# Kernel tuning notes

Hardware: AMD Instinct MI355X
Metric: run time of the kernel (lower is better)

The kernel has to match this reference:

```python
import jax, jax.numpy as jnp
import numpy as np

B, H, W, C = 2, 64, 64, 1024
L = H * W
HC, WC = 32, 32
NH, DH = 16, 64
NUM_REMAIN = 1638


def setup_inputs() -> dict:
    key = jax.random.key(0)
    ks = jax.random.split(key, 8)
    s = 1.0 / np.sqrt(C)
    x = jax.random.normal(ks[0], (B, L, C), jnp.float32)
    cached_x = jax.random.normal(ks[1], (B, HC, WC, C), jnp.float32)
    W_qkv = jax.random.normal(ks[2], (3 * C, C), jnp.float32) * s
    q_bias = jnp.zeros((C,), jnp.float32)
    v_bias = jnp.zeros((C,), jnp.float32)
    W_proj = jax.random.normal(ks[3], (C, C), jnp.float32) * s
    b_proj = jnp.zeros((C,), jnp.float32)
    scale_mul_log = jnp.full((1, NH, 1, 1), np.log(4.0), jnp.float32)
    # rope cache as (cos, sin) pairs over the flat token axis, DH//2 freqs
    ang = jax.random.uniform(ks[4], (L, DH // 2), jnp.float32) * (2 * np.pi)
    rope_grid = jnp.stack([jnp.cos(ang), jnp.sin(ang)], axis=0)  # (2, L, DH//2)
    return {"x": x, "cached_x": cached_x, "W_qkv": W_qkv, "q_bias": q_bias,
            "v_bias": v_bias, "W_proj": W_proj, "b_proj": b_proj,
            "scale_mul_log": scale_mul_log, "rope_grid": rope_grid,
            "num_remain": NUM_REMAIN}


def reference(x, cached_x, W_qkv, q_bias, v_bias, W_proj, b_proj,
              scale_mul_log, rope_grid, num_remain):
    Bx, Lx, Cx = x.shape
    # --- FastVAR token merge: MSE-to-spatial-mean selection (adaptive_avg_pool2d -> mean over L)
    mean_x = jnp.mean(x, axis=1, keepdims=True)                      # (B,1,C)
    mse = jnp.sum((x - mean_x) ** 2, axis=-1)                        # (B,L)
    idx = jnp.argsort(-mse, axis=1)[:, :num_remain]                  # (B,n) descending
    bix = jnp.arange(Bx)[:, None]
    xm = x[bix, idx]                                                 # (B,n,C) merged tokens
    # --- qkv projection with (q_bias, 0, v_bias)
    bias = jnp.concatenate([q_bias, jnp.zeros_like(q_bias), v_bias])
    qkv = (xm @ W_qkv.T + bias).reshape(Bx, -1, 3, NH, DH)
    qkv = qkv.transpose(2, 0, 3, 1, 4)                               # (3,B,H,n,dh)
    q, k, v = qkv[0], qkv[1], qkv[2]
    # --- cos attention: L2-normalize q,k; head-wise learned scale on q; sdpa scale = 1
    scale_mul = jnp.exp(jnp.minimum(scale_mul_log, jnp.log(100.0)))  # (1,NH,1,1)
    def l2n(t):
        return t / jnp.maximum(jnp.linalg.norm(t, axis=-1, keepdims=True), 1e-12)
    q = l2n(q) * scale_mul
    k = l2n(k)
    # --- 2D RoPE with per-sample gathered cache at the kept-token positions
    rc = rope_grid[:, idx, :]                                        # (2,B,n,DH//2)
    r0 = rc[0][:, None, :, :]                                        # (B,1,n,DH//2)
    r1 = rc[1][:, None, :, :]
    def rope(t):
        tp = t.reshape(*t.shape[:-1], DH // 2, 2)
        t0, t1 = tp[..., 0], tp[..., 1]
        return jnp.stack([r0 * t0 - r1 * t1, r1 * t0 + r0 * t1], axis=-1).reshape(t.shape)
    q = rope(q)
    k = rope(k)
    # --- attention over merged tokens
    attn = jax.nn.softmax(jnp.einsum('bhqd,bhkd->bhqk', q, k), axis=-1)
    o = jnp.einsum('bhqk,bhkd->bhqd', attn, v)                       # (B,H,n,dh)
    o = o.transpose(0, 2, 1, 3).reshape(Bx, -1, Cx)                  # (B,n,C)
    o = o @ W_proj.T + b_proj
    up = jnp.repeat(jnp.repeat(cached_x, 2, axis=1), 2, axis=2).reshape(Bx, Lx, Cx)
    out_full = up.at[bix, idx].set(o)
    return x + out_full
```

## Files before the change

kernel.cpp:

```cpp
#include <hip/hip_runtime.h>
#include <hip/hip_bf16.h>
#include <math.h>

#define BQ   2
#define LQ   4096
#define CQ   1024
#define NHQ  16
#define DHQ  64
#define KSEL 1638
#define KPAD 1664
#define MTOT (BQ*KSEL)
#define MPAD 3328

typedef short s16x8 __attribute__((ext_vector_type(8)));
typedef float fx4   __attribute__((ext_vector_type(4)));

#define MFMA16(a,b,c) __builtin_amdgcn_mfma_f32_16x16x32_bf16(a,b,c,0,0,0)

__device__ __forceinline__ float b2f(unsigned short u) {
  union { float f; unsigned int i; } cv; cv.i = ((unsigned int)u) << 16; return cv.f;
}
__device__ __forceinline__ unsigned short f2b(float f) {
  union { float f; unsigned int i; } cv; cv.f = f;
  unsigned int x = cv.i;
  return (unsigned short)((x + 0x7fffu + ((x >> 16) & 1u)) >> 16);
}
__device__ __forceinline__ unsigned int fbits(float f) {
  union { float f; unsigned int i; } cv; cv.f = f; return cv.i;
}
__device__ __forceinline__ void async16(const void* g, void* l) {
  __builtin_amdgcn_global_load_lds((const __attribute__((address_space(1))) void*)g,
                                   (__attribute__((address_space(3))) void*)l, 16, 0, 0);
}
__device__ __forceinline__ float fexp2(float x) {
#if __has_builtin(__builtin_amdgcn_exp2f)
  return __builtin_amdgcn_exp2f(x);
#else
  return __expf(x * 0.69314718055994531f);
#endif
}

__global__ __launch_bounds__(256) void k_cvt2(const float* __restrict__ wqkv,
                                              const float* __restrict__ wproj,
                                              unsigned short* __restrict__ wqb,
                                              unsigned short* __restrict__ wpb) {
  int i = blockIdx.x * 256 + threadIdx.x;
  const float* s; unsigned short* d; int off;
  if (i < 786432) { s = wqkv;  d = wqb; off = i; }
  else            { s = wproj; d = wpb; off = i - 786432; }
  float4 v = ((const float4*)s)[off];
  ushort4 o;
  o.x = f2b(v.x); o.y = f2b(v.y); o.z = f2b(v.z); o.w = f2b(v.w);
  ((ushort4*)d)[off] = o;
}

__global__ __launch_bounds__(256) void k_mean_part(const float* __restrict__ x,
                                                   double* __restrict__ part) {
  int bid = blockIdx.x;
  int cb = bid & 3, ch = (bid >> 2) & 31, b = bid >> 7;
  int c = cb * 256 + threadIdx.x;
  const float* p = x + ((size_t)b * LQ + (size_t)ch * 128) * CQ + c;
  double s = 0.0;
  for (int r = 0; r < 128; ++r) s += (double)p[(size_t)r * CQ];
  part[((size_t)b * 32 + ch) * CQ + c] = s;
}

__global__ __launch_bounds__(256) void k_mean_reduce(const double* __restrict__ part,
                                                     double* __restrict__ mean) {
  int g = blockIdx.x * 256 + threadIdx.x;
  int b = g >> 10, c = g & 1023;
  double s = 0.0;
  for (int ch = 0; ch < 32; ++ch) s += part[((size_t)b * 32 + ch) * CQ + c];
  mean[g] = s * (1.0 / 4096.0);
}

__global__ __launch_bounds__(256) void k_mse_base(const float* __restrict__ x,
                                                  const float* __restrict__ cached,
                                                  const double* __restrict__ mean,
                                                  double* __restrict__ mse,
                                                  float* __restrict__ out,
                                                  unsigned short* __restrict__ xb) {
  int bl = blockIdx.x; int b = bl >> 12, l = bl & 4095;
  int hh = l >> 6, ww = l & 63;
  size_t xoff = ((size_t)b * LQ + l) * CQ;
  size_t uoff = (((size_t)b * 32 + (hh >> 1)) * 32 + (ww >> 1)) * CQ;
  const double* mrow = mean + (size_t)b * CQ;
  int c0 = threadIdx.x * 4;
  float4 xv = *(const float4*)(x + xoff + c0);
  float4 uv = *(const float4*)(cached + uoff + c0);
  float4 ov;
  ov.x = xv.x + uv.x; ov.y = xv.y + uv.y; ov.z = xv.z + uv.z; ov.w = xv.w + uv.w;
  *(float4*)(out + xoff + c0) = ov;
  ushort4 xo;
  xo.x = f2b(xv.x); xo.y = f2b(xv.y); xo.z = f2b(xv.z); xo.w = f2b(xv.w);
  ((ushort4*)xb)[(xoff + c0) >> 2] = xo;
  double d0 = (double)xv.x - mrow[c0];
  double d1 = (double)xv.y - mrow[c0 + 1];
  double d2 = (double)xv.z - mrow[c0 + 2];
  double d3 = (double)xv.w - mrow[c0 + 3];
  double ss = d0 * d0 + d1 * d1 + d2 * d2 + d3 * d3;
  for (int o = 1; o < 64; o <<= 1) ss += __shfl_xor(ss, o);
  __shared__ double ws4[4];
  if ((threadIdx.x & 63) == 0) ws4[threadIdx.x >> 6] = ss;
  __syncthreads();
  if (threadIdx.x == 0) mse[(size_t)b * LQ + l] = ws4[0] + ws4[1] + ws4[2] + ws4[3];
}

__global__ __launch_bounds__(1024) void k_topk(const double* __restrict__ mse,
                                               int* __restrict__ idx_sel) {
  __shared__ unsigned long long u[4096];
  __shared__ unsigned int whist[16 * 257];
  __shared__ unsigned int wtot[4];
  __shared__ unsigned long long sh_prefix;
  __shared__ int sh_rem, sh_rem2, sh_bsel, sh_cnt, sh_eqcnt;
  __shared__ int eqbuf[256];
  int b = blockIdx.x, t = threadIdx.x;
  int wv = t >> 6, laneid = t & 63;
  for (int p = 0; p < 4; ++p) {
    int i = p * 1024 + t;
    u[i] = (unsigned long long)__double_as_longlong(mse[(size_t)b * LQ + i]);
  }
  if (t == 0) { sh_prefix = 0ULL; sh_rem = KSEL; sh_cnt = 0; sh_eqcnt = 0; }
  __syncthreads();
  for (int shift = 56; shift >= 0; shift -= 8) {
    for (int z = t; z < 16 * 257; z += 1024) whist[z] = 0u;
    __syncthreads();
    unsigned long long pref = sh_prefix;
#pragma unroll
    for (int p = 0; p < 4; ++p) {
      int i = p * 1024 + t;
      unsigned long long v = u[i];
      bool cand = (shift == 56) || ((v >> ((shift + 8) & 63)) == pref);
      if (cand) atomicAdd(&whist[wv * 257 + ((unsigned int)(v >> shift) & 255u)], 1u);
    }
    __syncthreads();
    unsigned int myc = 0, mysc = 0;
    if (t < 256) {
      unsigned int s = 0;
      int bin = 255 - t;
#pragma unroll
      for (int wvi = 0; wvi < 16; ++wvi) s += whist[wvi * 257 + bin];
      myc = s;
      mysc = myc;
#pragma unroll
      for (int o = 1; o < 64; o <<= 1) {
        unsigned int v2 = __shfl_up(mysc, o);
        if (laneid >= o) mysc += v2;
      }
      if (laneid == 63) wtot[wv] = mysc;
    }
    __syncthreads();
    if (t < 256) {
      unsigned int basep = 0;
      for (int wvi = 0; wvi < wv; ++wvi) basep += wtot[wvi];
      unsigned int incl = basep + mysc;
      unsigned int excl = incl - myc;
      unsigned int rem = (unsigned int)sh_rem;
      if (excl < rem && rem <= incl) {
        sh_bsel = 255 - t;
        sh_rem2 = (int)(rem - excl);
      }
    }
    __syncthreads();
    if (t == 0) {
      sh_prefix = (sh_prefix << 8) | (unsigned long long)sh_bsel;
      sh_rem = sh_rem2;
    }
    __syncthreads();
  }
  unsigned long long T = sh_prefix;
  int rem_eq = sh_rem;
#pragma unroll
  for (int p = 0; p < 4; ++p) {
    int i = p * 1024 + t;
    unsigned long long v = u[i];
    bool win = (v > T);
    unsigned long long mask = __ballot(win);
    int total = __popcll(mask);
    int base = 0;
    if (laneid == 0 && total > 0) base = atomicAdd(&sh_cnt, total);
    base = __shfl(base, 0);
    if (win) {
      int lpos = __popcll(mask & ((1ULL << laneid) - 1ULL));
      idx_sel[b * KPAD + base + lpos] = i;
    }
    if (v == T) {
      int e = atomicAdd(&sh_eqcnt, 1);
      if (e < 256) eqbuf[e] = i;
    }
  }
  __syncthreads();
  if (t == 0) {
    int n = sh_eqcnt; if (n > 256) n = 256;
    for (int a = 1; a < n; ++a) {
      int key = eqbuf[a]; int c = a - 1;
      while (c >= 0 && eqbuf[c] > key) { eqbuf[c + 1] = eqbuf[c]; --c; }
      eqbuf[c + 1] = key;
    }
    int base = sh_cnt;
    for (int a = 0; a < rem_eq && a < n; ++a) idx_sel[b * KPAD + base + a] = eqbuf[a];
    for (int a = KSEL; a < KPAD; ++a) idx_sel[b * KPAD + a] = 0;
  }
}

__global__ __launch_bounds__(256) void k_gemmA(const unsigned short* __restrict__ Asrc,
                                               const unsigned short* __restrict__ Bmat,
                                               const int* __restrict__ idx_sel,
                                               unsigned short* __restrict__ Cbf) {
  int bm = blockIdx.x % 26, bn = blockIdx.x / 26;
  int tid = threadIdx.x;
  int w = tid >> 6, lane = tid & 63, quad = lane >> 4, l15 = lane & 15;
  int wm = w & 1, wn = w >> 1;
  __shared__ __align__(16) unsigned char sm[2][16384];

  const unsigned short* gA[2];
  const unsigned short* gB[2];
#pragma unroll
  for (int p = 0; p < 2; ++p) {
    int e = p * 256 + tid; int row = e >> 2, kc = e & 3;
    int m = bm * 128 + row; if (m >= MTOT) m = MTOT - 1;
    int bb = m / KSEL; int ii = m - bb * KSEL;
    int lsel = idx_sel[bb * KPAD + ii];
    gA[p] = Asrc + ((size_t)bb * LQ + lsel) * CQ + kc * 8;
    gB[p] = Bmat + (size_t)(bn * 128 + row) * CQ + kc * 8;
  }

  fx4 acc[4][4];
#pragma unroll
  for (int a = 0; a < 4; ++a)
#pragma unroll
    for (int c = 0; c < 4; ++c) acc[a][c] = (fx4){0.f, 0.f, 0.f, 0.f};

#define STAGE_A(buf, it) do { int ke = (it) * 32;                                   \
    _Pragma("unroll")                                                               \
    for (int p = 0; p < 2; ++p) {                                                   \
      async16(gA[p] + ke, sm[buf] + p * 4096 + w * 1024);                           \
      async16(gB[p] + ke, sm[buf] + 8192 + p * 4096 + w * 1024);                    \
    } } while (0)

  STAGE_A(0, 0);
  for (int it = 0; it < 32; ++it) {
    int cur = it & 1;
    if (it < 31) STAGE_A(cur ^ 1, it + 1);
    if (it < 31) asm volatile("s_waitcnt vmcnt(4)");
    else         asm volatile("s_waitcnt vmcnt(0)");
    __builtin_amdgcn_s_barrier();
    const unsigned char* smb = sm[cur];
    s16x8 af[4], bf[4];
#pragma unroll
    for (int mt = 0; mt < 4; ++mt)
      af[mt] = *(const s16x8*)(smb + ((wm * 64 + mt * 16 + l15) * 64 + quad * 16));
#pragma unroll
    for (int nt = 0; nt < 4; ++nt)
      bf[nt] = *(const s16x8*)(smb + 8192 + ((wn * 64 + nt * 16 + l15) * 64 + quad * 16));
#pragma unroll
    for (int mt = 0; mt < 4; ++mt)
#pragma unroll
      for (int nt = 0; nt < 4; ++nt)
        acc[mt][nt] = MFMA16(af[mt], bf[nt], acc[mt][nt]);
    __builtin_amdgcn_s_barrier();
  }
#undef STAGE_A

#pragma unroll
  for (int mt = 0; mt < 4; ++mt)
#pragma unroll
    for (int nt = 0; nt < 4; ++nt) {
      int n = bn * 128 + wn * 64 + nt * 16 + l15;
      int mbase = bm * 128 + wm * 64 + mt * 16 + quad * 4;
      fx4 vv = acc[mt][nt];
#pragma unroll
      for (int r = 0; r < 4; ++r) {
        int m = mbase + r;
        if (m < MTOT) Cbf[(size_t)m * 3072 + n] = f2b(vv[r]);
      }
    }
}

__global__ __launch_bounds__(256) void k_gemmB(const unsigned short* __restrict__ Asrc,
                                               const unsigned short* __restrict__ Bmat,
                                               const int* __restrict__ idx_sel,
                                               float* __restrict__ Cf,
                                               const float* __restrict__ xin,
                                               const float* __restrict__ bproj) {
  int bid = blockIdx.x;
  int swz = (bid & 7) * 104 + (bid >> 3);
  int bm = swz % 52, bn = swz / 52;
  int tid = threadIdx.x;
  int w = tid >> 6, lane = tid & 63, quad = lane >> 4, l15 = lane & 15;
  int wm = w & 1, wn = w >> 1;
  __shared__ __align__(16) unsigned char sm[2][16384];

  const unsigned short* g4[4];
#pragma unroll
  for (int p = 0; p < 4; ++p) {
    int e = (p & 1) * 256 + tid; int row = e >> 3, kc = e & 7;
    if (p < 2) {
      int m = bm * 64 + row; if (m >= MTOT) m = MTOT - 1;
      int bb = m / KSEL; int ii = m - bb * KSEL;
      g4[p] = Asrc + ((size_t)bb * KPAD + ii) * CQ + kc * 8;
    } else {
      g4[p] = Bmat + (size_t)(bn * 64 + row) * CQ + kc * 8;
    }
  }

  fx4 acc[2][2];
#pragma unroll
  for (int a = 0; a < 2; ++a)
#pragma unroll
    for (int c = 0; c < 2; ++c) acc[a][c] = (fx4){0.f, 0.f, 0.f, 0.f};

#define STAGE_B(buf, it) do { int ke = (it) * 64;                                   \
    _Pragma("unroll")                                                               \
    for (int p = 0; p < 4; ++p)                                                     \
      async16(g4[p] + ke, sm[buf] + p * 4096 + w * 1024);                           \
    } while (0)

  STAGE_B(0, 0);
  for (int it = 0; it < 16; ++it) {
    int cur = it & 1;
    if (it < 15) STAGE_B(cur ^ 1, it + 1);
    if (it < 15) asm volatile("s_waitcnt vmcnt(4)");
    else         asm volatile("s_waitcnt vmcnt(0)");
    __builtin_amdgcn_s_barrier();
    const unsigned char* smb = sm[cur];
#pragma unroll
    for (int kk = 0; kk < 2; ++kk) {
      s16x8 af[2], bf2[2];
#pragma unroll
      for (int mt = 0; mt < 2; ++mt)
        af[mt] = *(const s16x8*)(smb + ((wm * 32 + mt * 16 + l15) * 64 + kk * 32 + quad * 8) * 2);
#pragma unroll
      for (int nt = 0; nt < 2; ++nt)
        bf2[nt] = *(const s16x8*)(smb + 8192 + ((wn * 32 + nt * 16 + l15) * 64 + kk * 32 + quad * 8) * 2);
#pragma unroll
      for (int mt = 0; mt < 2; ++mt)
#pragma unroll
        for (int nt = 0; nt < 2; ++nt)
          acc[mt][nt] = MFMA16(af[mt], bf2[nt], acc[mt][nt]);
    }
    __builtin_amdgcn_s_barrier();
  }
#undef STAGE_B

#pragma unroll
  for (int mt = 0; mt < 2; ++mt)
#pragma unroll
    for (int nt = 0; nt < 2; ++nt) {
      int n = bn * 64 + wn * 32 + nt * 16 + l15;
      int mbase = bm * 64 + wm * 32 + mt * 16 + quad * 4;
      fx4 vv = acc[mt][nt];
      float bp = bproj[n];
#pragma unroll
      for (int r = 0; r < 4; ++r) {
        int m = mbase + r;
        if (m < MTOT) {
          int bb = m / KSEL; int ii = m - bb * KSEL;
          int lsel = idx_sel[bb * KPAD + ii];
          size_t off = ((size_t)bb * LQ + lsel) * CQ + n;
          Cf[off] = xin[off] + vv[r] + bp;
        }
      }
    }
}

__global__ __launch_bounds__(256) void k_normrope(const unsigned short* __restrict__ qkv,
                                                  const int* __restrict__ idx_sel,
                                                  const float* __restrict__ qbias,
                                                  const float* __restrict__ vbias,
                                                  const float* __restrict__ sml,
                                                  const float* __restrict__ rope,
                                                  unsigned short* __restrict__ qo,
                                                  unsigned short* __restrict__ ko,
                                                  unsigned short* __restrict__ vt) {
  int bid = blockIdx.x;
  int tile = bid % 26; int h = (bid / 26) & 15; int b = bid / (26 * 16);
  int tid = threadIdx.x; int w = tid >> 6; int d = tid & 63;
  __shared__ unsigned short vtile[64 * 68];
  float scale = expf(fminf(sml[h], 4.6051702f)) * 1.4426950408889634f;
  float qb = qbias[h * 64 + d];
  float vb = vbias[h * 64 + d];
  for (int pass = 0; pass < 16; ++pass) {
    int il = pass * 4 + w;
    int i = tile * 64 + il;
    float vraw = 0.f;
    if (i < KSEL) {
      int lsel = idx_sel[b * KPAD + i];
      size_t base = ((size_t)(b * KSEL + i)) * 3072 + h * 64 + d;
      int tt = d >> 1;
      float r0 = rope[(size_t)lsel * 32 + tt];
      float r1 = rope[(size_t)LQ * 32 + (size_t)lsel * 32 + tt];
      float qv = b2f(qkv[base]) + qb;
      float ss = qv * qv;
      for (int o = 1; o < 64; o <<= 1) ss += __shfl_xor(ss, o);
      float qn = qv / fmaxf(sqrtf(ss), 1e-12f) * scale;
      float qp = __shfl_xor(qn, 1);
      float qr = (d & 1) ? (r1 * qp + r0 * qn) : (r0 * qn - r1 * qp);
      qo[((size_t)(b * NHQ + h) * KPAD + i) * 64 + d] = f2b(qr);
      float kv = b2f(qkv[base + 1024]);
      float ks = kv * kv;
      for (int o = 1; o < 64; o <<= 1) ks += __shfl_xor(ks, o);
      float kn = kv / fmaxf(sqrtf(ks), 1e-12f);
      float kp = __shfl_xor(kn, 1);
      float kr = (d & 1) ? (r1 * kp + r0 * kn) : (r0 * kn - r1 * kp);
      ko[((size_t)(b * NHQ + h) * KPAD + i) * 64 + d] = f2b(kr);
      vraw = b2f(qkv[base + 2048]) + vb;
    }
    vtile[d * 68 + il] = f2b(vraw);
  }
  __syncthreads();
  int row = tid >> 2, c0 = (tid & 3) * 16;
  s16x8 o0, o1;
#pragma unroll
  for (int jj = 0; jj < 8; ++jj) {
    o0[jj] = (short)vtile[row * 68 + c0 + jj];
    o1[jj] = (short)vtile[row * 68 + c0 + 8 + jj];
  }
  size_t doff = ((size_t)((b * NHQ + h) * 64 + row)) * KPAD + (size_t)tile * 64 + c0;
  *(s16x8*)(vt + doff) = o0;
  *(s16x8*)(vt + doff + 8) = o1;
}

__global__ __launch_bounds__(256, 4) void k_attn(const unsigned short* __restrict__ qb,
                                                 const unsigned short* __restrict__ kb,
                                                 const unsigned short* __restrict__ vtb,
                                                 const float* __restrict__ sml,
                                                 unsigned short* __restrict__ pO,
                                                 float* __restrict__ pl) {
  int qt = blockIdx.x; int bh = blockIdx.y; int part = blockIdx.z;
  int b = bh >> 4, h = bh & 15;
  int t0 = part * 13, t1 = t0 + 13;
  int q0 = qt * 128;
  int tid = threadIdx.x, w = tid >> 6, lane = tid & 63, quad = lane >> 4, l15 = lane & 15;
  float M = __expf(fminf(sml[h], 4.6051702f)) * 1.4426950408889634f;
  __shared__ __align__(16) unsigned short Kt[64 * 72];
  __shared__ __align__(16) unsigned short Vt[64 * 72];
  __shared__ __align__(16) unsigned short Pq[4][32 * 72];
  unsigned short* Pw = Pq[w];
  const unsigned short* qbase = qb + (size_t)(b * NHQ + h) * KPAD * 64;
  const unsigned short* kbase = kb + (size_t)(b * NHQ + h) * KPAD * 64;
  const unsigned short* vbase = vtb + (size_t)(b * NHQ + h) * 64 * KPAD;

  s16x8 qf[2][2];
#pragma unroll
  for (int qtile = 0; qtile < 2; ++qtile)
#pragma unroll
    for (int kb2 = 0; kb2 < 2; ++kb2) {
      int row = q0 + w * 32 + qtile * 16 + l15;
      qf[qtile][kb2] = *(const s16x8*)(qbase + (size_t)row * 64 + kb2 * 32 + quad * 8);
    }

  float lsum[2] = {0.f, 0.f};
  fx4 oacc[2][4];
#pragma unroll
  for (int qtile = 0; qtile < 2; ++qtile)
#pragma unroll
    for (int dt = 0; dt < 4; ++dt) oacc[qtile][dt] = (fx4){0.f, 0.f, 0.f, 0.f};

  for (int t = t0; t < t1; ++t) {
    int j0 = t * 64;
    bool tail = (j0 + 64 > KSEL);
    __syncthreads();
#pragma unroll
    for (int p = 0; p < 2; ++p) {
      int e = p * 256 + tid; int row = e >> 3, kc = e & 7;
      *(s16x8*)(Kt + row * 72 + kc * 8) =
          *(const s16x8*)(kbase + (size_t)(j0 + row) * 64 + kc * 8);
      *(s16x8*)(Vt + row * 72 + kc * 8) =
          *(const s16x8*)(vbase + (size_t)row * KPAD + j0 + kc * 8);
    }
    __syncthreads();

    fx4 sacc[2][4];
#pragma unroll
    for (int qtile = 0; qtile < 2; ++qtile)
#pragma unroll
      for (int jj = 0; jj < 4; ++jj) sacc[qtile][jj] = (fx4){0.f, 0.f, 0.f, 0.f};
#pragma unroll
    for (int jj = 0; jj < 4; ++jj) {
      int jl = jj * 16 + l15;
      s16x8 kf0 = *(const s16x8*)(Kt + jl * 72 + quad * 8);
      s16x8 kf1 = *(const s16x8*)(Kt + jl * 72 + 32 + quad * 8);
      sacc[0][jj] = MFMA16(kf0, qf[0][0], sacc[0][jj]);
      sacc[1][jj] = MFMA16(kf0, qf[1][0], sacc[1][jj]);
      sacc[0][jj] = MFMA16(kf1, qf[0][1], sacc[0][jj]);
      sacc[1][jj] = MFMA16(kf1, qf[1][1], sacc[1][jj]);
    }
#pragma unroll
    for (int qtile = 0; qtile < 2; ++qtile)
#pragma unroll
      for (int jj = 0; jj < 4; ++jj) {
        int jbase = j0 + jj * 16 + quad * 4;
        fx4 sv = sacc[qtile][jj];
        float p0 = fexp2(sv[0] - M);
        float p1 = fexp2(sv[1] - M);
        float p2 = fexp2(sv[2] - M);
        float p3 = fexp2(sv[3] - M);
        if (tail) {
          if (jbase + 0 >= KSEL) p0 = 0.f;
          if (jbase + 1 >= KSEL) p1 = 0.f;
          if (jbase + 2 >= KSEL) p2 = 0.f;
          if (jbase + 3 >= KSEL) p3 = 0.f;
        }
        lsum[qtile] += (p0 + p1) + (p2 + p3);
        unsigned int lo = (fbits(p1) & 0xffff0000u) | (fbits(p0) >> 16);
        unsigned int hi = (fbits(p3) & 0xffff0000u) | (fbits(p2) >> 16);
        *(uint2*)(Pw + (qtile * 16 + l15) * 72 + jj * 16 + quad * 4) =
            make_uint2(lo, hi);
      }
#pragma unroll
    for (int js = 0; js < 2; ++js) {
      s16x8 pf0 = *(const s16x8*)(Pw + l15 * 72 + js * 32 + quad * 8);
      s16x8 pf1 = *(const s16x8*)(Pw + (16 + l15) * 72 + js * 32 + quad * 8);
#pragma unroll
      for (int dt = 0; dt < 4; ++dt) {
        s16x8 vf = *(const s16x8*)(Vt + (dt * 16 + l15) * 72 + js * 32 + quad * 8);
        oacc[0][dt] = MFMA16(pf0, vf, oacc[0][dt]);
        oacc[1][dt] = MFMA16(pf1, vf, oacc[1][dt]);
      }
    }
  }

#pragma unroll
  for (int qtile = 0; qtile < 2; ++qtile) {
    float s = lsum[qtile];
    s += __shfl_xor(s, 16);
    s += __shfl_xor(s, 32);
    lsum[qtile] = s;
  }

  size_t pbase = (((size_t)part * 2 + b) * NHQ + h) * KPAD;
#pragma unroll
  for (int qtile = 0; qtile < 2; ++qtile) {
    int gqb = q0 + w * 32 + qtile * 16;
    if (quad == 0) pl[pbase + gqb + l15] = lsum[qtile];
  }

#pragma unroll
  for (int qtile = 0; qtile < 2; ++qtile)
#pragma unroll
    for (int dt = 0; dt < 4; ++dt)
#pragma unroll
      for (int r = 0; r < 4; ++r)
        Pw[(qtile * 16 + quad * 4 + r) * 72 + dt * 16 + l15] = f2b(oacc[qtile][dt][r]);
#pragma unroll
  for (int pass = 0; pass < 4; ++pass) {
    int row = pass * 8 + (lane >> 3), chunk = lane & 7;
    s16x8 vv = *(const s16x8*)(Pw + row * 72 + chunk * 8);
    *(s16x8*)(pO + (pbase + q0 + w * 32 + row) * 64 + chunk * 8) = vv;
  }
}

__global__ __launch_bounds__(256) void k_comb(const unsigned short* __restrict__ pO,
                                              const float* __restrict__ pl,
                                              unsigned short* __restrict__ ob) {
  size_t g = (size_t)blockIdx.x * 256 + threadIdx.x;
  int d = (int)(g & 63);
  size_t row = g >> 6;
  int gq = (int)(row % KPAD);
  int bhh = (int)(row / KPAD);
  int b = bhh >> 4, h = bhh & 15;
  float oa = b2f(pO[g]);
  float obv = b2f(pO[g + 3407872]);
  float la = pl[row], lb = pl[row + 53248];
  float o = (oa + obv) / (la + lb);
  ob[((size_t)(b * KPAD + gq)) * CQ + h * 64 + d] = f2b(o);
}

extern "C" void kernel_launch(void* const* d_in, const int* in_sizes, int n_in,
                              void* d_out, int out_size, void* d_ws, size_t ws_size,
                              hipStream_t stream) {
  const float* x      = (const float*)d_in[0];
  const float* cached = (const float*)d_in[1];
  const float* wqkv   = (const float*)d_in[2];
  const float* qbias  = (const float*)d_in[3];
  const float* vbias  = (const float*)d_in[4];
  const float* wproj  = (const float*)d_in[5];
  const float* bproj  = (const float*)d_in[6];
  const float* sml    = (const float*)d_in[7];
  const float* rope   = (const float*)d_in[8];
  float* out = (float*)d_out;
  char* ws = (char*)d_ws;

  double* meanpart        = (double*)(ws);
  double* mean            = (double*)(ws + 524288);
  double* mse             = (double*)(ws + 540672);
  int* idx_sel            = (int*)(ws + 606208);
  unsigned short* x_bf    = (unsigned short*)(ws + 619520);
  unsigned short* wqkv_bf = (unsigned short*)(ws + 17396736);
  unsigned short* qkv     = (unsigned short*)(ws + 23688192);
  unsigned short* pO      = (unsigned short*)(ws + 619520);
  float* pl               = (float*)(ws + 14251008);
  unsigned short* wproj_bf= (unsigned short*)(ws + 44135424);
  unsigned short* qo      = (unsigned short*)(ws + 46232576);
  unsigned short* ko      = (unsigned short*)(ws + 53048320);
  unsigned short* vt      = (unsigned short*)(ws + 59864064);
  unsigned short* ob      = (unsigned short*)(ws + 66679808);

  hipLaunchKernelGGL(k_cvt2, dim3(4096), dim3(256), 0, stream, wqkv, wproj,
                     wqkv_bf, wproj_bf);
  hipLaunchKernelGGL(k_mean_part, dim3(256), dim3(256), 0, stream, x, meanpart);
  hipLaunchKernelGGL(k_mean_reduce, dim3(8), dim3(256), 0, stream, meanpart, mean);
  hipLaunchKernelGGL(k_mse_base, dim3(8192), dim3(256), 0, stream, x, cached, mean, mse,
                     out, x_bf);
  hipLaunchKernelGGL(k_topk, dim3(BQ), dim3(1024), 0, stream, mse, idx_sel);
  hipLaunchKernelGGL(k_gemmA, dim3(26 * 24), dim3(256), 0, stream,
                     x_bf, wqkv_bf, idx_sel, qkv);
  hipLaunchKernelGGL(k_normrope, dim3(26 * 16 * BQ), dim3(256), 0, stream,
                     qkv, idx_sel, qbias, vbias, sml, rope, qo, ko, vt);
  hipLaunchKernelGGL(k_attn, dim3(13, BQ * NHQ, 2), dim3(256), 0, stream,
                     qo, ko, vt, sml, pO, pl);
  hipLaunchKernelGGL(k_comb, dim3(13312), dim3(256), 0, stream, pO, pl, ob);
  hipLaunchKernelGGL(k_gemmB, dim3(832), dim3(256), 0, stream,
                     ob, wproj_bf, idx_sel, out, x, bproj);
}
```

Before: 285.8 us.

## Prefetch next K/V tile into registers and raise MFMA wave priority

The attention kernel now loads the next 64-row K and V tile from global memory into registers while the current tile is computed, then writes the registers to shared memory after a raw s_barrier. This is a register-level double buffer that hides global load latency behind the MFMA work. It also wraps the two MFMA loops in s_setprio(1)/s_setprio(0) so waves doing matrix work get scheduling priority. The cost is extra VGPRs for the prefetch buffers, which can lower occupancy, and the hand-written waitcnt and barrier sequence has to keep the LDS stores and reads correctly ordered.

```diff
diff --git a/kernel.cpp b/kernel.cpp
--- a/kernel.cpp
+++ b/kernel.cpp
@@ -441,6 +441,9 @@
   const unsigned short* kbase = kb + (size_t)(b * NHQ + h) * KPAD * 64;
   const unsigned short* vbase = vtb + (size_t)(b * NHQ + h) * 64 * KPAD;
 
+  int r0 = tid >> 3, c0 = tid & 7;
+  int r1 = 32 + r0, c1 = c0;
+
   s16x8 qf[2][2];
 #pragma unroll
   for (int qtile = 0; qtile < 2; ++qtile)
@@ -457,25 +460,39 @@
 #pragma unroll
     for (int dt = 0; dt < 4; ++dt) oacc[qtile][dt] = (fx4){0.f, 0.f, 0.f, 0.f};
 
+  s16x8 kn0, kn1, vn0, vn1;
+  {
+    int j0 = t0 * 64;
+    kn0 = *(const s16x8*)(kbase + (size_t)(j0 + r0) * 64 + c0 * 8);
+    kn1 = *(const s16x8*)(kbase + (size_t)(j0 + r1) * 64 + c1 * 8);
+    vn0 = *(const s16x8*)(vbase + (size_t)r0 * KPAD + j0 + c0 * 8);
+    vn1 = *(const s16x8*)(vbase + (size_t)r1 * KPAD + j0 + c1 * 8);
+  }
+
   for (int t = t0; t < t1; ++t) {
     int j0 = t * 64;
     bool tail = (j0 + 64 > KSEL);
-    __syncthreads();
-#pragma unroll
-    for (int p = 0; p < 2; ++p) {
-      int e = p * 256 + tid; int row = e >> 3, kc = e & 7;
-      *(s16x8*)(Kt + row * 72 + kc * 8) =
-          *(const s16x8*)(kbase + (size_t)(j0 + row) * 64 + kc * 8);
-      *(s16x8*)(Vt + row * 72 + kc * 8) =
-          *(const s16x8*)(vbase + (size_t)row * KPAD + j0 + kc * 8);
-    }
-    __syncthreads();
+    __builtin_amdgcn_s_barrier();
+    *(s16x8*)(Kt + r0 * 72 + c0 * 8) = kn0;
+    *(s16x8*)(Kt + r1 * 72 + c1 * 8) = kn1;
+    *(s16x8*)(Vt + r0 * 72 + c0 * 8) = vn0;
+    *(s16x8*)(Vt + r1 * 72 + c1 * 8) = vn1;
+    if (t + 1 < t1) {
+      int jn = (t + 1) * 64;
+      kn0 = *(const s16x8*)(kbase + (size_t)(jn + r0) * 64 + c0 * 8);
+      kn1 = *(const s16x8*)(kbase + (size_t)(jn + r1) * 64 + c1 * 8);
+      vn0 = *(const s16x8*)(vbase + (size_t)r0 * KPAD + jn + c0 * 8);
+      vn1 = *(const s16x8*)(vbase + (size_t)r1 * KPAD + jn + c1 * 8);
+    }
+    asm volatile("s_waitcnt lgkmcnt(0)" ::: "memory");
+    __builtin_amdgcn_s_barrier();
 
     fx4 sacc[2][4];
 #pragma unroll
     for (int qtile = 0; qtile < 2; ++qtile)
 #pragma unroll
       for (int jj = 0; jj < 4; ++jj) sacc[qtile][jj] = (fx4){0.f, 0.f, 0.f, 0.f};
+    __builtin_amdgcn_s_setprio(1);
 #pragma unroll
     for (int jj = 0; jj < 4; ++jj) {
       int jl = jj * 16 + l15;
@@ -486,6 +503,7 @@
       sacc[0][jj] = MFMA16(kf1, qf[0][1], sacc[0][jj]);
       sacc[1][jj] = MFMA16(kf1, qf[1][1], sacc[1][jj]);
     }
+    __builtin_amdgcn_s_setprio(0);
 #pragma unroll
     for (int qtile = 0; qtile < 2; ++qtile)
 #pragma unroll
@@ -508,6 +526,7 @@
         *(uint2*)(Pw + (qtile * 16 + l15) * 72 + jj * 16 + quad * 4) =
             make_uint2(lo, hi);
       }
+    __builtin_amdgcn_s_setprio(1);
 #pragma unroll
     for (int js = 0; js < 2; ++js) {
       s16x8 pf0 = *(const s16x8*)(Pw + l15 * 72 + js * 32 + quad * 8);
@@ -519,6 +538,7 @@
         oacc[1][dt] = MFMA16(pf1, vf, oacc[1][dt]);
       }
     }
+    __builtin_amdgcn_s_setprio(0);
   }
 
 #pragma unroll
```

Result: no change. 289.2 us (+1.2%).
